# Kernel optimization log

Measured on AMD Instinct MI355X. Metric: run time of the kernel, lower is better.

## Reference

```python
import jax, jax.numpy as jnp
import numpy as np

Z, N, K, W = 131072, 64, 64, 32


def setup_inputs() -> dict:
    key = jax.random.key(0)
    k1, k2, k3 = jax.random.split(key, 3)
    features = jax.random.normal(k1, (Z, N), dtype=jnp.float32)
    # dense realization of the CG-derived mixing tensor 'wkij'
    mixing_matrix = jax.random.normal(k2, (W, K, N, N), dtype=jnp.float32) * 0.05
    weight = jax.random.normal(k3, (W,), dtype=jnp.float32)
    return {"features": features, "mixing_matrix": mixing_matrix, "weight": weight}


def reference(features, mixing_matrix, weight):
    # torch: einsum('w,wkij,zi,zj->zk', weight, mixing_matrix, features, features)
    # Contract the small path axis w first -> [K, N, N] (cheap, tiny output),
    # then the bilinear square over z. einsum chooses a GEMM-style path; the
    # [Z, N, N] outer-product side is the memory-bound part.
    M = jnp.einsum('w,wkij->kij', weight, mixing_matrix)  # [K, N, N]
    out = jnp.einsum('kij,zi,zj->zk', M, features, features)  # [Z, K]
    return out
```

## Files before the change

### kernel.cpp

```cpp
#include <hip/hip_runtime.h>
#include <stdint.h>

typedef __attribute__((ext_vector_type(8))) _Float16 half8;
typedef __attribute__((ext_vector_type(2))) _Float16 h2;
typedef __attribute__((ext_vector_type(4))) float f32x4;

#define NCHUNK 32

static __device__ __forceinline__ unsigned short f2h(float f) {
  return __builtin_bit_cast(unsigned short, (_Float16)f);
}
static __device__ __forceinline__ void gload16(const void* g, void* l) {
  __builtin_amdgcn_global_load_lds((const __attribute__((address_space(1))) void*)g,
                                   (__attribute__((address_space(3))) void*)l, 16, 0, 0);
}

__global__ __launch_bounds__(1024) void prep_kernel(const float* __restrict__ mix,
                                                    const float* __restrict__ wgt,
                                                    unsigned short* __restrict__ Bp) {
  __shared__ float T[4096];
  const int k   = blockIdx.x;
  const int tid = threadIdx.x;
  const float4* m4 = (const float4*)mix + (size_t)k * 1024 + tid;
  float4 a = {0.f, 0.f, 0.f, 0.f};
#pragma unroll
  for (int w = 0; w < 32; ++w) {
    const float s = wgt[w];
    const float4 v = m4[(size_t)w * 65536];
    a.x += s * v.x; a.y += s * v.y; a.z += s * v.z; a.w += s * v.w;
  }
  *(float4*)(&T[tid * 4]) = a;
  __syncthreads();
  ushort4 r;
#pragma unroll
  for (int e = 0; e < 4; ++e) {
    const int t = tid * 4 + e, i = t >> 6, j = t & 63;
    float v;
    if (i < j)       v = T[t] + T[(j << 6) | i];
    else if (i == j) v = T[t];
    else             v = 0.f;
    ((unsigned short*)&r)[e] = f2h(v);
  }
  ((ushort4*)Bp)[k * 1024 + tid] = r;
}

__global__ __launch_bounds__(512, 4) void gemm_kernel(const float* __restrict__ X,
                                                      const unsigned short* __restrict__ Bp,
                                                      float* __restrict__ out) {
  __shared__ unsigned short ldsB[3][64 * 128];
  __shared__ unsigned short sH[2][2][256];

  const int tid  = threadIdx.x;
  const int lane = tid & 63;
  const int wv   = tid >> 6;
  const int wz   = wv >> 1;
  const int wk   = wv & 1;
  const int m    = lane & 15;
  const int q    = lane >> 4;
  const int zblk = blockIdx.x * 256;

  auto stageB = [&](int ct, int bf) {
#pragma unroll
    for (int it = 0; it < 2; ++it) {
      const int seg = wv * 2 + it;
      const int row = seg * 4 + (lane >> 4);
      const int u   = (lane & 15) ^ (row & 15);
      gload16(Bp + (size_t)row * 4096 + ct * 128 + u * 8,
              &ldsB[bf][seg * 512]);
    }
  };

  auto publishS = [&](int bf, float2 xp) {
    if (tid < 256) {
      const int d  = (tid >> 6) * 32 + (tid & 15) * 2 + ((tid >> 5) & 1);
      const int hf = (tid >> 4) & 1;
      sH[bf][0][d * 2 + hf] = f2h(xp.x);
      sH[bf][1][d * 2 + hf] = f2h(xp.y);
    }
  };

  stageB(0, 0);
  stageB(1, 1);
  {
    float2 xp0 = {0.f, 0.f};
    if (tid < 256) xp0 = *(const float2*)(X + (size_t)(zblk + tid) * 64);
    publishS(0, xp0);
  }

  h2 jh[4][8];
  {
    const float4* X4g = (const float4*)X;
#pragma unroll
    for (int f = 0; f < 4; ++f) {
      const int zg = zblk + wz * 64 + f * 16 + m;
#pragma unroll
      for (int h = 0; h < 2; ++h) {
        const float4 a = X4g[zg * 16 + h * 8 + q * 2];
        const float4 b = X4g[zg * 16 + h * 8 + q * 2 + 1];
        jh[f][h * 4 + 0] = h2{(_Float16)a.x, (_Float16)a.y};
        jh[f][h * 4 + 1] = h2{(_Float16)a.z, (_Float16)a.w};
        jh[f][h * 4 + 2] = h2{(_Float16)b.x, (_Float16)b.y};
        jh[f][h * 4 + 3] = h2{(_Float16)b.z, (_Float16)b.w};
      }
    }
  }

  f32x4 acc[4][2];
#pragma unroll
  for (int f = 0; f < 4; ++f)
#pragma unroll
    for (int g = 0; g < 2; ++g) acc[f][g] = f32x4{0.f, 0.f, 0.f, 0.f};

  __syncthreads();

  int bufc = 0;
  for (int c = 0; c < NCHUNK; ++c) {
    const int cn = (c + 1) & (NCHUNK - 1);
    float2 spre = {0.f, 0.f};
    if (tid < 256)
      spre = *(const float2*)(X + (size_t)(zblk + tid) * 64 + cn * 2);
    int bs = bufc + 2; if (bs >= 3) bs -= 3;
    stageB((c + 2) & (NCHUNK - 1), bs);

    const unsigned short* Bl = &ldsB[bufc][0];
    const bool full = (c < 16);

#pragma unroll
    for (int il = 0; il < 2; ++il) {
      const uint2 sv = *(const uint2*)(&sH[c & 1][il][wz * 64 + m * 4]);
      h2 s2f[4];
      s2f[0] = __builtin_bit_cast(h2, __builtin_amdgcn_perm(sv.x, sv.x, 0x01000100u));
      s2f[1] = __builtin_bit_cast(h2, __builtin_amdgcn_perm(sv.x, sv.x, 0x03020302u));
      s2f[2] = __builtin_bit_cast(h2, __builtin_amdgcn_perm(sv.y, sv.y, 0x01000100u));
      s2f[3] = __builtin_bit_cast(h2, __builtin_amdgcn_perm(sv.y, sv.y, 0x03020302u));
      const unsigned short* base = Bl + (wk * 32 + m) * 128;
      const int u0 = ((il << 3) + q) ^ m;
      const int u1 = ((il << 3) + 4 + q) ^ m;
      half8 bf[2][2];
      if (full) {
        bf[0][0] = *(const half8*)(const void*)(base + u0 * 8);
        bf[0][1] = *(const half8*)(const void*)(base + 16 * 128 + u0 * 8);
      }
      bf[1][0] = *(const half8*)(const void*)(base + u1 * 8);
      bf[1][1] = *(const half8*)(const void*)(base + 16 * 128 + u1 * 8);
      __builtin_amdgcn_sched_barrier(0);

      __builtin_amdgcn_s_barrier();
      asm volatile("s_waitcnt lgkmcnt(0)" ::: "memory");
      __builtin_amdgcn_sched_barrier(0);

      __builtin_amdgcn_s_setprio(1);
      auto cluster = [&](int h, half8 b0, half8 b1) {
#pragma unroll
        for (int f = 0; f < 4; ++f) {
          union { unsigned u[4]; half8 v; } A;
#pragma unroll
          for (int e = 0; e < 4; ++e) {
            const h2 pr = s2f[f] * jh[f][h * 4 + e];
            A.u[e] = __builtin_bit_cast(unsigned, pr);
          }
          acc[f][0] = __builtin_amdgcn_mfma_f32_16x16x32_f16(A.v, b0, acc[f][0], 0, 0, 0);
          acc[f][1] = __builtin_amdgcn_mfma_f32_16x16x32_f16(A.v, b1, acc[f][1], 0, 0, 0);
        }
      };
      if (full) cluster(0, bf[0][0], bf[0][1]);
      cluster(1, bf[1][0], bf[1][1]);
      __builtin_amdgcn_s_setprio(0);

      if (il == 1) {
        publishS(cn & 1, spre);
        asm volatile("s_waitcnt vmcnt(2)" ::: "memory");
        asm volatile("s_waitcnt lgkmcnt(0)" ::: "memory");
      }
      __builtin_amdgcn_s_barrier();
      __builtin_amdgcn_sched_barrier(0);
    }
    bufc = (bufc + 1 == 3) ? 0 : bufc + 1;
  }

#pragma unroll
  for (int f = 0; f < 4; ++f) {
    const int zr = zblk + wz * 64 + f * 16 + q * 4;
#pragma unroll
    for (int g = 0; g < 2; ++g)
#pragma unroll
      for (int r = 0; r < 4; ++r)
        out[(size_t)(zr + r) * 64 + wk * 32 + g * 16 + m] = acc[f][g][r];
  }
}

extern "C" void kernel_launch(void* const* d_in, const int* in_sizes, int n_in,
                              void* d_out, int out_size, void* d_ws, size_t ws_size,
                              hipStream_t stream) {
  const float* X   = (const float*)d_in[0];
  const float* mix = (const float*)d_in[1];
  const float* wgt = (const float*)d_in[2];
  float* out = (float*)d_out;
  unsigned short* Bp = (unsigned short*)d_ws;

  prep_kernel<<<64, 1024, 0, stream>>>(mix, wgt, Bp);
  gemm_kernel<<<512, 512, 0, stream>>>(X, Bp, out);
}
```

Before: 164.2 us.

## Load B fragments directly from global into registers, drop LDS staging and barriers

The prep kernel now writes the symmetrized fp16 mixing matrix in an MFMA-fragment-ready layout, so the GEMM kernel can load B operands straight from global/L2 into registers with a 3-deep register ring. LDS staging, the per-step block barriers and the shared scalar broadcast are removed. The per-row scaling factors are taken with cross-lane shuffles from the already-held feature registers. Blocks shrink to 256 threads covering 128 rows, with each wave computing all 64 output columns. The aim is to eliminate barrier stalls and LDS traffic, at the cost of every wave re-reading B from cache and higher register pressure.

Measured after the change: 158.6 us. 3.4% less time.

```diff
diff --git a/kernel.cpp b/kernel.cpp
--- a/kernel.cpp
+++ b/kernel.cpp
@@ -5,14 +5,8 @@
 typedef __attribute__((ext_vector_type(2))) _Float16 h2;
 typedef __attribute__((ext_vector_type(4))) float f32x4;
 
-#define NCHUNK 32
-
 static __device__ __forceinline__ unsigned short f2h(float f) {
   return __builtin_bit_cast(unsigned short, (_Float16)f);
-}
-static __device__ __forceinline__ void gload16(const void* g, void* l) {
-  __builtin_amdgcn_global_load_lds((const __attribute__((address_space(1))) void*)g,
-                                   (__attribute__((address_space(3))) void*)l, 16, 0, 0);
 }
 
 __global__ __launch_bounds__(1024) void prep_kernel(const float* __restrict__ mix,
@@ -41,58 +35,33 @@
     else             v = 0.f;
     ((unsigned short*)&r)[e] = f2h(v);
   }
-  ((ushort4*)Bp)[k * 1024 + tid] = r;
+  const int t0  = tid * 4;
+  const int off = ((t0 >> 5) * 4 + (k >> 4)) * 512 + ((t0 >> 3) & 3) * 128
+                + (k & 15) * 8 + (t0 & 7);
+  *(ushort4*)(Bp + off) = r;
 }
 
-__global__ __launch_bounds__(512, 4) void gemm_kernel(const float* __restrict__ X,
+static __device__ __forceinline__ void blk_coords(int idx, int& c, int& il, int& h) {
+  if (idx < 64) { c = idx >> 2; il = (idx >> 1) & 1; h = idx & 1; }
+  else { const int r = idx - 64; c = 16 + (r >> 1); il = r & 1; h = 1; }
+}
+
+__global__ __launch_bounds__(256, 3) void gemm_kernel(const float* __restrict__ X,
                                                       const unsigned short* __restrict__ Bp,
                                                       float* __restrict__ out) {
-  __shared__ unsigned short ldsB[3][64 * 128];
-  __shared__ unsigned short sH[2][2][256];
-
   const int tid  = threadIdx.x;
   const int lane = tid & 63;
   const int wv   = tid >> 6;
-  const int wz   = wv >> 1;
-  const int wk   = wv & 1;
   const int m    = lane & 15;
   const int q    = lane >> 4;
-  const int zblk = blockIdx.x * 256;
+  const int zblk = blockIdx.x * 128;
 
-  auto stageB = [&](int ct, int bf) {
-#pragma unroll
-    for (int it = 0; it < 2; ++it) {
-      const int seg = wv * 2 + it;
-      const int row = seg * 4 + (lane >> 4);
-      const int u   = (lane & 15) ^ (row & 15);
-      gload16(Bp + (size_t)row * 4096 + ct * 128 + u * 8,
-              &ldsB[bf][seg * 512]);
-    }
-  };
-
-  auto publishS = [&](int bf, float2 xp) {
-    if (tid < 256) {
-      const int d  = (tid >> 6) * 32 + (tid & 15) * 2 + ((tid >> 5) & 1);
-      const int hf = (tid >> 4) & 1;
-      sH[bf][0][d * 2 + hf] = f2h(xp.x);
-      sH[bf][1][d * 2 + hf] = f2h(xp.y);
-    }
-  };
-
-  stageB(0, 0);
-  stageB(1, 1);
-  {
-    float2 xp0 = {0.f, 0.f};
-    if (tid < 256) xp0 = *(const float2*)(X + (size_t)(zblk + tid) * 64);
-    publishS(0, xp0);
-  }
-
-  h2 jh[4][8];
+  h2 jh[2][8];
   {
     const float4* X4g = (const float4*)X;
 #pragma unroll
-    for (int f = 0; f < 4; ++f) {
-      const int zg = zblk + wz * 64 + f * 16 + m;
+    for (int f = 0; f < 2; ++f) {
+      const int zg = zblk + wv * 32 + f * 16 + m;
 #pragma unroll
       for (int h = 0; h < 2; ++h) {
         const float4 a = X4g[zg * 16 + h * 8 + q * 2];
@@ -105,87 +74,68 @@
     }
   }
 
-  f32x4 acc[4][2];
+  f32x4 acc[2][4];
 #pragma unroll
-  for (int f = 0; f < 4; ++f)
+  for (int f = 0; f < 2; ++f)
 #pragma unroll
-    for (int g = 0; g < 2; ++g) acc[f][g] = f32x4{0.f, 0.f, 0.f, 0.f};
+    for (int g = 0; g < 4; ++g) acc[f][g] = f32x4{0.f, 0.f, 0.f, 0.f};
 
-  __syncthreads();
+  const uint4* Bv = (const uint4*)Bp;
+  uint4 bbuf[3][4];
+  auto loadB = [&](int idx, uint4* dst) {
+    int c, il, h; blk_coords(idx, c, il, h);
+    const int s4 = (c * 4 + il * 2 + h) * 4;
+#pragma unroll
+    for (int g = 0; g < 4; ++g) dst[g] = Bv[(s4 + g) * 64 + lane];
+  };
 
-  int bufc = 0;
-  for (int c = 0; c < NCHUNK; ++c) {
-    const int cn = (c + 1) & (NCHUNK - 1);
-    float2 spre = {0.f, 0.f};
-    if (tid < 256)
-      spre = *(const float2*)(X + (size_t)(zblk + tid) * 64 + cn * 2);
-    int bs = bufc + 2; if (bs >= 3) bs -= 3;
-    stageB((c + 2) & (NCHUNK - 1), bs);
-
-    const unsigned short* Bl = &ldsB[bufc][0];
-    const bool full = (c < 16);
+  loadB(0, bbuf[0]);
+  loadB(1, bbuf[1]);
 
 #pragma unroll
-    for (int il = 0; il < 2; ++il) {
-      const uint2 sv = *(const uint2*)(&sH[c & 1][il][wz * 64 + m * 4]);
-      h2 s2f[4];
-      s2f[0] = __builtin_bit_cast(h2, __builtin_amdgcn_perm(sv.x, sv.x, 0x01000100u));
-      s2f[1] = __builtin_bit_cast(h2, __builtin_amdgcn_perm(sv.x, sv.x, 0x03020302u));
-      s2f[2] = __builtin_bit_cast(h2, __builtin_amdgcn_perm(sv.y, sv.y, 0x01000100u));
-      s2f[3] = __builtin_bit_cast(h2, __builtin_amdgcn_perm(sv.y, sv.y, 0x03020302u));
-      const unsigned short* base = Bl + (wk * 32 + m) * 128;
-      const int u0 = ((il << 3) + q) ^ m;
-      const int u1 = ((il << 3) + 4 + q) ^ m;
-      half8 bf[2][2];
-      if (full) {
-        bf[0][0] = *(const half8*)(const void*)(base + u0 * 8);
-        bf[0][1] = *(const half8*)(const void*)(base + 16 * 128 + u0 * 8);
+  for (int idx = 0; idx < 96; ++idx) {
+    if (idx + 2 < 96) loadB(idx + 2, bbuf[(idx + 2) % 3]);
+
+    int c, il, h; blk_coords(idx, c, il, h);
+    const int i    = 2 * c + il;
+    const int hs   = i >> 5;
+    const int qs   = (i >> 3) & 3;
+    const int es   = (i & 7) >> 1;
+    const int half = i & 1;
+    h2 s2f[2];
+#pragma unroll
+    for (int f = 0; f < 2; ++f) {
+      const int du = __shfl((int)__builtin_bit_cast(unsigned, jh[f][hs * 4 + es]),
+                            qs * 16 + m, 64);
+      const unsigned uu = (unsigned)du;
+      s2f[f] = __builtin_bit_cast(h2, __builtin_amdgcn_perm(uu, uu,
+                                   half ? 0x03020302u : 0x01000100u));
+    }
+
+    const uint4* bc = bbuf[idx % 3];
+#pragma unroll
+    for (int f = 0; f < 2; ++f) {
+      union { unsigned u[4]; half8 v; } A;
+#pragma unroll
+      for (int e = 0; e < 4; ++e) {
+        const h2 pr = s2f[f] * jh[f][h * 4 + e];
+        A.u[e] = __builtin_bit_cast(unsigned, pr);
       }
-      bf[1][0] = *(const half8*)(const void*)(base + u1 * 8);
-      bf[1][1] = *(const half8*)(const void*)(base + 16 * 128 + u1 * 8);
-      __builtin_amdgcn_sched_barrier(0);
-
-      __builtin_amdgcn_s_barrier();
-      asm volatile("s_waitcnt lgkmcnt(0)" ::: "memory");
-      __builtin_amdgcn_sched_barrier(0);
-
-      __builtin_amdgcn_s_setprio(1);
-      auto cluster = [&](int h, half8 b0, half8 b1) {
 #pragma unroll
-        for (int f = 0; f < 4; ++f) {
-          union { unsigned u[4]; half8 v; } A;
-#pragma unroll
-          for (int e = 0; e < 4; ++e) {
-            const h2 pr = s2f[f] * jh[f][h * 4 + e];
-            A.u[e] = __builtin_bit_cast(unsigned, pr);
-          }
-          acc[f][0] = __builtin_amdgcn_mfma_f32_16x16x32_f16(A.v, b0, acc[f][0], 0, 0, 0);
-          acc[f][1] = __builtin_amdgcn_mfma_f32_16x16x32_f16(A.v, b1, acc[f][1], 0, 0, 0);
-        }
-      };
-      if (full) cluster(0, bf[0][0], bf[0][1]);
-      cluster(1, bf[1][0], bf[1][1]);
-      __builtin_amdgcn_s_setprio(0);
-
-      if (il == 1) {
-        publishS(cn & 1, spre);
-        asm volatile("s_waitcnt vmcnt(2)" ::: "memory");
-        asm volatile("s_waitcnt lgkmcnt(0)" ::: "memory");
-      }
-      __builtin_amdgcn_s_barrier();
-      __builtin_amdgcn_sched_barrier(0);
+      for (int g = 0; g < 4; ++g)
+        acc[f][g] = __builtin_amdgcn_mfma_f32_16x16x32_f16(
+            A.v, __builtin_bit_cast(half8, bc[g]), acc[f][g], 0, 0, 0);
     }
-    bufc = (bufc + 1 == 3) ? 0 : bufc + 1;
   }
 
 #pragma unroll
-  for (int f = 0; f < 4; ++f) {
-    const int zr = zblk + wz * 64 + f * 16 + q * 4;
+  for (int f = 0; f < 2; ++f) {
+    const int zr = zblk + wv * 32 + f * 16 + q * 4;
 #pragma unroll
-    for (int g = 0; g < 2; ++g)
+    for (int g = 0; g < 4; ++g)
 #pragma unroll
       for (int r = 0; r < 4; ++r)
-        out[(size_t)(zr + r) * 64 + wk * 32 + g * 16 + m] = acc[f][g][r];
+        out[(size_t)(zr + r) * 64 + g * 16 + m] = acc[f][g][r];
   }
 }
 
@@ -199,5 +149,5 @@
   unsigned short* Bp = (unsigned short*)d_ws;
 
   prep_kernel<<<64, 1024, 0, stream>>>(mix, wgt, Bp);
-  gemm_kernel<<<512, 512, 0, stream>>>(X, Bp, out);
+  gemm_kernel<<<1024, 256, 0, stream>>>(X, Bp, out);
 }
```
